# Kernel optimization log

Hardware: AMD Instinct MI355X
Metric: run time of the kernel (lower is better)

The kernel has to match this reference:

```python
import jax, jax.numpy as jnp
import numpy as np

BS, C, T = 16, 256, 768
PATCH = 12
NPATCH = T // PATCH            # 64 patches; 63 sequential update steps
FF, HEADS = 256, 4             # ff_dim = 2**ceil(log2(C)) = 256, divisible by heads
HD = FF // HEADS
TOPK = 3
ALPHA = 0.5
EPS = 1e-5                     # BatchNorm eps (eval mode, running stats mean=0, var=1)
NEG = -1000000000.0


def _bn(x2d, g, b):
    # eval-mode BatchNorm1d with default running stats (mean=0, var=1)
    return x2d * (g / np.float32(np.sqrt(1.0 + EPS))) + b


def _gelu(x):
    return jax.nn.gelu(x, approximate=False)  # torch F.gelu default = exact erf


def setup_inputs() -> dict:
    key = jax.random.key(0)
    ks = jax.random.split(key, 8)
    s = 0.05
    return {
        "x": jax.random.normal(ks[0], (BS, C, T), jnp.float32),
        "g0": jnp.ones((C * T,), jnp.float32), "b0": jnp.zeros((C * T,), jnp.float32),
        "g1": jnp.ones((C * PATCH,), jnp.float32), "b1": jnp.zeros((C * PATCH,), jnp.float32),
        "g2": jnp.ones((C * PATCH,), jnp.float32), "b2": jnp.zeros((C * PATCH,), jnp.float32),
        "W_agg": jax.random.normal(ks[1], (PATCH, PATCH), jnp.float32) * s,
        "b_agg": jnp.zeros((PATCH,), jnp.float32),
        "We": jax.random.normal(ks[2], (FF,), jnp.float32) * s,      # Linear(1, ff) weight[:,0]
        "be": jnp.zeros((FF,), jnp.float32),
        "Wq": jax.random.normal(ks[3], (FF, FF), jnp.float32) * s, "bq": jnp.zeros((FF,), jnp.float32),
        "Wk": jax.random.normal(ks[4], (FF, FF), jnp.float32) * s, "bk": jnp.zeros((FF,), jnp.float32),
        "Wv": jax.random.normal(ks[5], (FF, FF), jnp.float32) * s, "bv": jnp.zeros((FF,), jnp.float32),
        "Wm1": jax.random.normal(ks[6], (FF, FF), jnp.float32) * s, "bm1": jnp.zeros((FF,), jnp.float32),
        "Wm2": jax.random.normal(ks[7], (FF,), jnp.float32) * s,     # Linear(ff, 1) weight[0,:]
        "bm2": jnp.zeros((1,), jnp.float32),
    }


def reference(x, g0, b0, g1, b1, g2, b2, W_agg, b_agg, We, be,
              Wq, bq, Wk, bk, Wv, bv, Wm1, bm1, Wm2, bm2):
    # outer BatchNorm over flattened [bs, C*T]
    xn = _bn(x.reshape(BS, -1), g0, b0).reshape(BS, C, T)
    xp = xn.reshape(BS, C, NPATCH, PATCH).transpose(2, 0, 1, 3)  # [NP, bs, C, P]
    out0 = xp[0]

    def step(prev, xt):  # prev, xt: [bs, C, P]
        inp = _bn(prev.reshape(BS, -1), g1, b1).reshape(BS, C, PATCH)
        inp = _gelu(inp @ W_agg.T + b_agg)           # agg over patch dim (dropout=eval no-op)
        res = inp + xt                               # [bs, C, P]
        t = _bn(res.reshape(BS, -1), g2, b2).reshape(BS, C, PATCH).transpose(0, 2, 1)  # [bs,P,C]
        h = t[..., None] * We + be                   # channel_embed: [bs, P, C, FF]

        def proj(W, bvec):
            y = h @ W.T + bvec
            return y.reshape(BS, PATCH, C, HEADS, HD).transpose(0, 1, 3, 2, 4)  # [bs,P,H,C,hd]

        q, k, v = proj(Wq, bq), proj(Wk, bk), proj(Wv, bv)
        attn = jnp.einsum('bphcd,bphed->bphce', q, k) / np.float32(np.sqrt(HD))  # [bs,P,H,C,C]
        # top-k mask over channel-neighbor axis (scatter of top-k indices)
        flat = attn.reshape(-1, C)
        _, idx = jax.lax.top_k(flat, TOPK)
        rows = jnp.arange(flat.shape[0])[:, None]
        mask = jnp.zeros(flat.shape, bool).at[rows, idx].set(True).reshape(attn.shape)
        attn = jax.nn.softmax(jnp.where(mask, attn, NEG), axis=-1)
        hn = jnp.einsum('bphce,bphed->bphcd', attn, v).transpose(0, 1, 3, 2, 4).reshape(BS, PATCH, C, FF)
        z = _gelu(hn @ Wm1.T + bm1) @ Wm2 + bm2      # msg_mlp -> [bs, P, C]
        new = res + ALPHA * z.transpose(0, 2, 1)     # [bs, C, P]
        return new, new

    _, outs = jax.lax.scan(jax.checkpoint(step), out0, xp[1:])
    out = jnp.concatenate([out0[None], outs], axis=0)       # [NP, bs, C, P]
    return out.transpose(1, 2, 0, 3).reshape(BS, C, T)
```

## Files before the change

### kernel.cpp

```cpp
#include <hip/hip_runtime.h>
#include <math.h>

typedef unsigned int u32;
typedef unsigned long long u64;

#define BSZ   16
#define CCH   256
#define TT    768
#define PT    12
#define NPN   64
#define NH    4
#define NSL   4
#define GRID  (BSZ*NSL)
#define THR   768

#define WS_A    0
#define WS_CCF  4
#define WS_WAGG 80
#define WS_BAGG 224
#define WS_G1T  256
#define WS_B1T  3328
#define WS_G2T  6400
#define WS_B2T  9472
#define WS_S1Q  12544
#define WS_S1CQ 12800
#define WS_S1K  13056
#define WS_S1V  13312
#define WS_S1CV 13568
#define WS_M    13824
#define WS_CM1  14848
#define WS_EXF  16384
#define WS_XN   32768

#define INVSF 0.9999950000374996f
#define K2F   0.3989422804014327f

__device__ __forceinline__ float med3f(float a, float b, float c){
  return fmaxf(fminf(a,b), fminf(fmaxf(a,b), c));
}
__device__ __forceinline__ float gelu_fast(float v){
  float av = fabsf(v);
  if (__builtin_expect(av > 1.0f, 0))
    return 0.5f * v * (1.0f + erff(v * 0.7071067811865475f));
  float t = v * v;
  float r = 1.3319545e-06f;
  r = fmaf(r, t, -1.8889312e-05f);
  r = fmaf(r, t,  2.3086939e-04f);
  r = fmaf(r, t, -2.3746564e-03f);
  r = fmaf(r, t,  1.9947114e-02f);
  r = fmaf(r, t, -1.3298076e-01f);
  r = fmaf(r, t,  7.9788456e-01f);
  float a = 0.5f * v;
  return fmaf(a * v, r, a);
}
__device__ __forceinline__ float exp_t3(float x){
  float t = fmaf(x, 0.3333333333f, 1.0f);
  t = fmaf(x * 0.5f, t, 1.0f);
  return fmaf(x, t, 1.0f);
}
__device__ __forceinline__ float rdlane(float v, int lane){
  return __int_as_float(__builtin_amdgcn_readlane(__float_as_int(v), lane));
}
__device__ __forceinline__ void tstore(u64* p, u32 tag, float v){
  u64 w = ((u64)tag << 32) | (u64)(u32)__float_as_uint(v);
  __hip_atomic_store(p, w, __ATOMIC_RELAXED, __HIP_MEMORY_SCOPE_AGENT);
}
__device__ __forceinline__ float tpoll(const u64* p, u32 tag){
  u64 v;
  do { v = __hip_atomic_load(p, __ATOMIC_RELAXED, __HIP_MEMORY_SCOPE_AGENT); }
  while ((u32)(v >> 32) != tag);
  return __uint_as_float((u32)v);
}

#define TRIPLE_STAGE(CTRL) { \
  float o1 = __int_as_float(__builtin_amdgcn_update_dpp(ni, __float_as_int(t1), CTRL, 0xf, 0xf, false)); \
  float o2 = __int_as_float(__builtin_amdgcn_update_dpp(ni, __float_as_int(t2), CTRL, 0xf, 0xf, false)); \
  float o3 = __int_as_float(__builtin_amdgcn_update_dpp(ni, __float_as_int(t3), CTRL, 0xf, 0xf, false)); \
  float yy = fminf(t1,o1), xx = fmaxf(t2,o2); \
  t1 = fmaxf(t1,o1); \
  float n3 = med3f(yy, xx, fmaxf(t3,o3)); \
  t2 = fmaxf(yy,xx); t3 = n3; }

__global__ __launch_bounds__(1024) void precompute1_kernel(
    const float* __restrict__ x,   const float* __restrict__ g0,
    const float* __restrict__ b0,
    const float* __restrict__ gg1, const float* __restrict__ bb1,
    const float* __restrict__ gg2, const float* __restrict__ bb2,
    const float* __restrict__ Wagg, const float* __restrict__ bagg,
    const float* __restrict__ We,  const float* __restrict__ be,
    const float* __restrict__ Wq,  const float* __restrict__ bq,
    const float* __restrict__ Wk,
    const float* __restrict__ Wv,  const float* __restrict__ bv,
    float* __restrict__ ws)
{
  const int tid = threadIdx.x;

  if (blockIdx.x < 768) {
    __shared__ float tile[4][32*33];
    const int tau = blockIdx.x*4 + (tid >> 8);
    const int b   = tau / 192;
    const int rem = tau - b*192;
    const int t0  = (rem % 24) * 32;
    const int c0  = (rem / 24) * 32;
    const int id8 = tid & 255;
    float* tl = &tile[tid >> 8][0];
    const long xb = (long)b * (CCH*TT);
    {
      const int c  = id8 >> 3;
      const int tq = (id8 & 7) << 2;
      const int ict = (c0 + c)*TT + t0 + tq;
      const float4 xv4 = *reinterpret_cast<const float4*>(x  + xb + ict);
      const float4 gv4 = *reinterpret_cast<const float4*>(g0 + ict);
      const float4 bv4 = *reinterpret_cast<const float4*>(b0 + ict);
      float* tr = tl + c*33 + tq;
      tr[0] = fmaf(xv4.x, gv4.x*INVSF, bv4.x);
      tr[1] = fmaf(xv4.y, gv4.y*INVSF, bv4.y);
      tr[2] = fmaf(xv4.z, gv4.z*INVSF, bv4.z);
      tr[3] = fmaf(xv4.w, gv4.w*INVSF, bv4.w);
    }
    __syncthreads();
    {
      const int tt = id8 >> 3;
      const int cq = (id8 & 7) << 2;
      float4 o;
      o.x = tl[(cq    )*33 + tt];
      o.y = tl[(cq + 1)*33 + tt];
      o.z = tl[(cq + 2)*33 + tt];
      o.w = tl[(cq + 3)*33 + tt];
      *reinterpret_cast<float4*>(ws + WS_XN + ((long)b*TT + t0 + tt)*CCH + c0 + cq) = o;
    }
    return;
  }

  __shared__ float We_s[CCH], be_s[CCH];
  const int lane = tid & 63;
  const int w    = tid >> 6;
  if (tid < CCH) { We_s[tid] = We[tid]; be_s[tid] = be[tid]; }
  __syncthreads();

  const int f = (blockIdx.x - 768)*16 + w;
  float aq=0.f, cqa=0.f, ak=0.f, av=0.f, cva=0.f;
  #pragma unroll
  for (int k2 = 0; k2 < 4; ++k2) {
    int j = lane + 64*k2;
    float wev = We_s[j], bev = be_s[j];
    float q1 = Wq[f*CCH + j]; aq += q1*wev; cqa += q1*bev;
    float k1 = Wk[f*CCH + j]; ak += k1*wev;
    float v1 = Wv[f*CCH + j]; av += v1*wev; cva += v1*bev;
  }
  for (int ofs = 1; ofs < 64; ofs <<= 1) {
    aq += __shfl_xor(aq, ofs);  cqa += __shfl_xor(cqa, ofs);
    ak += __shfl_xor(ak, ofs);
    av += __shfl_xor(av, ofs);  cva += __shfl_xor(cva, ofs);
  }
  if (lane == 0) {
    ws[WS_S1Q  + f] = aq;
    ws[WS_S1CQ + f] = cqa + bq[f];
    ws[WS_S1K  + f] = ak;
    ws[WS_S1V  + f] = av;
    ws[WS_S1CV + f] = cva + bv[f];
  }

  if (blockIdx.x == 768) {
    for (int i = tid; i < PT*CCH; i += 1024) {
      int j = i >> 8, c = i & 255;
      ws[WS_G1T + i] = gg1[c*PT + j] * INVSF;
      ws[WS_B1T + i] = bb1[c*PT + j];
      ws[WS_G2T + i] = gg2[c*PT + j] * INVSF;
      ws[WS_B2T + i] = bb2[c*PT + j];
    }
    if (tid < PT*PT) ws[WS_WAGG + tid] = Wagg[tid];
    if (tid < PT)    ws[WS_BAGG + tid] = bagg[tid];
  }
}

__global__ __launch_bounds__(1024) void precompute2_kernel(
    const float* __restrict__ Wm1, const float* __restrict__ bm1,
    float* __restrict__ ws)
{
  const int tid  = threadIdx.x;
  const int lane = tid & 63;
  const int w    = tid >> 6;

  if (blockIdx.x < 16) {
    __shared__ float wv_l[CCH], cv_l[CCH];
    if (tid < CCH) { wv_l[tid] = ws[WS_S1V + tid]; cv_l[tid] = ws[WS_S1CV + tid]; }
    __syncthreads();
    const int g = blockIdx.x*16 + w;
    float mk0=0.f, mk1=0.f, mk2=0.f, mk3=0.f, ca=0.f;
    #pragma unroll
    for (int k2 = 0; k2 < 4; ++k2) {
      int j = lane + 64*k2;
      float wv1 = Wm1[g*CCH + j];
      float pm = wv1 * wv_l[j];
      if (k2 == 0) mk0 = pm; else if (k2 == 1) mk1 = pm; else if (k2 == 2) mk2 = pm; else mk3 = pm;
      ca += wv1 * cv_l[j];
    }
    for (int ofs = 1; ofs < 64; ofs <<= 1) {
      mk0 += __shfl_xor(mk0, ofs); mk1 += __shfl_xor(mk1, ofs);
      mk2 += __shfl_xor(mk2, ofs); mk3 += __shfl_xor(mk3, ofs);
      ca  += __shfl_xor(ca,  ofs);
    }
    if (lane == 0) {
      ws[WS_M + g*4+0] = mk0; ws[WS_M + g*4+1] = mk1;
      ws[WS_M + g*4+2] = mk2; ws[WS_M + g*4+3] = mk3;
      ws[WS_CM1 + g] = ca + bm1[g];
    }
    return;
  }

  if (tid < NH*64) {
    const int f = w*64 + lane;
    float a  = ws[WS_S1Q + f] * ws[WS_S1K + f];
    float cc = ws[WS_S1CQ + f] * ws[WS_S1K + f];
    for (int ofs = 1; ofs < 64; ofs <<= 1) { a += __shfl_xor(a, ofs); cc += __shfl_xor(cc, ofs); }
    if (lane == 0) { ws[WS_A + w] = a * 0.125f; ws[WS_CCF + w] = cc * 0.125f; }
  }
}

__device__ __forceinline__ float poly_acc(const float* __restrict__ ws,
                                          const float* __restrict__ Wm2,
                                          int m, int l)
{
  float acc = 0.f;
  #pragma unroll
  for (int k = 0; k < 4; ++k) {
    const int g = l + 64*k;
    const float W  = Wm2[g];
    const float cg = ws[WS_CM1 + g];
    float val;
    if (m == 0)      val = fmaf(K2F*cg, cg, 0.5f*cg);
    else if (m <= 4) val = fmaf(2.f*K2F, cg, 0.5f) * ws[WS_M + g*4 + (m-1)];
    else {
      const int u  = m - 5;
      const int hh = (u<4)?0:(u<7)?1:(u<9)?2:3;
      const int kk = (u<4)?u:(u<7)?(u-3):(u<9)?(u-5):3;
      val = K2F * ws[WS_M + g*4 + hh] * ws[WS_M + g*4 + kk] * ((hh==kk)?1.f:2.f);
    }
    acc += W * val;
  }
  for (int ofs = 1; ofs < 64; ofs <<= 1) acc += __shfl_xor(acc, ofs);
  return acc;
}

__global__ __launch_bounds__(THR) void main_kernel(
    float* __restrict__ ws, float* __restrict__ out,
    const float* __restrict__ Wm2, const float* __restrict__ bm2)
{
  const int blk   = blockIdx.x;
  const int b     = blk & 15;
  const int slice = blk >> 4;
  const int c0    = slice * 64;
  const int tid   = threadIdx.x;
  const int p     = tid >> 6;
  const int l     = tid & 63;

  __shared__ float tmp_sh[2][PT][64];
  __shared__ float o_buf[3*PT][69];
  __shared__ float C_lds[15];

  {
    float c = poly_acc(ws, Wm2, p, l);
    if (l == 0) C_lds[p] = c + (p == 0 ? bm2[0] : 0.f);
    if (p < 3) {
      float c2 = poly_acc(ws, Wm2, p + 12, l);
      if (l == 0) C_lds[p + 12] = c2;
    }
  }

  const int cg = c0 + l;
  const float g1r = ws[WS_G1T + p*CCH + cg];
  const float b1r = ws[WS_B1T + p*CCH + cg];
  const float g2r = ws[WS_G2T + p*CCH + cg];
  const float b2r = ws[WS_B2T + p*CCH + cg];
  float waggr[PT];
  #pragma unroll
  for (int j = 0; j < PT; ++j) waggr[j] = ws[WS_WAGG + p*PT + j];
  const float baggp = ws[WS_BAGG + p];
  float Ah[NH], Ch[NH];
  #pragma unroll
  for (int h = 0; h < NH; ++h) { Ah[h] = ws[WS_A + h]; Ch[h] = ws[WS_CCF + h]; }
  __syncthreads();

  float C15[15];
  #pragma unroll
  for (int m = 0; m < 15; ++m)
    C15[m] = __int_as_float(__builtin_amdgcn_readfirstlane(__float_as_int(C_lds[m])));

  u64* exBase = ((u64*)(ws + WS_EXF)) + (size_t)(b*PT + p) * (NSL*8);
  u64* exMine = exBase + slice*8;

  const long xb  = (long)b * (CCH*TT);
  const float* xnb = ws + WS_XN + (long)b*(TT*CCH);
  const int ni = __float_as_int(-1e30f);

  const int cfl  = tid / PT;
  const int part = tid - cfl*PT;
  float* outP = out + xb + (long)(c0 + cfl)*TT + part;
  const float* obP = &o_buf[0][0] + part*69 + cfl;

  float st = xnb[(long)(0*PT + p)*CCH + cg];
  o_buf[p][l] = st;

  const float* xp = xnb + (long)p*CCH + cg;
  int fl = 0;
  int wr = 1;

  for (int t = 1; t < NPN; ++t) {
    const int par = t & 1;
    const u32 tag = (u32)t;
    xp += PT*CCH;
    const float xv = *xp;

    tmp_sh[par][p][l] = fmaf(st, g1r, b1r);
    __syncthreads();

    float acc = baggp;
    #pragma unroll
    for (int j = 0; j < PT; ++j)
      acc = fmaf(tmp_sh[par][j][l], waggr[j], acc);
    float res = gelu_fast(acc) + xv;
    float s   = fmaf(res, g2r, b2r);

    const int src = (l & 31) << 1;
    float v0 = __shfl(s, src), v1 = __shfl(s, src + 1);
    float FBloc = 0.f;
    if (slice == 0)
      FBloc = (rdlane(s, 0) + rdlane(s, 1) + rdlane(s, 2)) * (1.0f/3.0f);
    if (l >= 32) { v0 = -v0; v1 = -v1; }
    float t1 = fmaxf(v0, v1), t2 = fminf(v0, v1), t3 = -1e30f;
    TRIPLE_STAGE(0x111);
    TRIPLE_STAGE(0x112);
    TRIPLE_STAGE(0x114);
    TRIPLE_STAGE(0x118);
    TRIPLE_STAGE(0x142);
    const float lt1 = rdlane(t1, 31), lt2 = rdlane(t2, 31), lt3 = rdlane(t3, 31);
    const float lu1 = rdlane(t1, 63), lu2 = rdlane(t2, 63), lu3 = rdlane(t3, 63);

    {
      float sw = (l == 0) ? lt1 : (l == 1) ? lt2 : (l == 2) ? lt3
               : (l == 3) ? lu1 : (l == 4) ? lu2 : lu3;
      if (l < 6) tstore(exMine + l, tag, sw);
      if (slice == 0 && l == 6) tstore(exMine + 6, tag, FBloc);
    }

    if (t >= 2) {
      const int tt = t - 2;
      outP[tt*PT] = obP[fl*(PT*69)];
      fl = (fl + 1 < 3) ? fl + 1 : 0;
    }

    float pv = 0.f;
    if (l < 18) {
      int pj = l / 6, word = l - pj*6;
      int pslice = pj + (pj >= slice);
      pv = tpoll(exBase + pslice*8 + word, tag);
    } else if (l == 18 && slice != 0) {
      pv = tpoll(exBase + 6, tag);
    }

    float T1 = lt1, T2 = lt2, T3 = lt3;
    float U1 = lu1, U2 = lu2, U3 = lu3;
    #pragma unroll
    for (int j = 0; j < 3; ++j) {
      const float q1 = rdlane(pv, 6*j),     q2 = rdlane(pv, 6*j + 1), q3 = rdlane(pv, 6*j + 2);
      const float r1 = rdlane(pv, 6*j + 3), r2 = rdlane(pv, 6*j + 4), r3 = rdlane(pv, 6*j + 5);
      float x1 = fminf(T1, q1), y1 = fmaxf(T2, q2);
      T1 = fmaxf(T1, q1);
      float nT3 = med3f(x1, y1, fmaxf(T3, q3));
      T2 = fmaxf(x1, y1); T3 = nT3;
      float x2 = fminf(U1, r1), y2 = fmaxf(U2, r2);
      U1 = fmaxf(U1, r1);
      float nU3 = med3f(x2, y2, fmaxf(U3, r3));
      U2 = fmaxf(x2, y2); U3 = nU3;
    }
    const float FB = (slice == 0) ? FBloc : rdlane(pv, 18);
    const float B1 = -U1, B2 = -U2, B3 = -U3;
    const float Td2 = T2 - T1, Td3 = T3 - T1;
    const float Bd2 = B2 - B1, Bd3 = B3 - B1;

    float S1v[NH];
    #pragma unroll
    for (int h = 0; h < NH; ++h) {
      float alpha = fmaf(Ah[h], s, Ch[h]);
      bool pos = alpha > 0.0f;
      float v1s = pos ? T1 : B1;
      float v2s = pos ? T2 : B2;
      float v3s = pos ? T3 : B3;
      float d2 = pos ? Td2 : Bd2;
      float d3 = pos ? Td3 : Bd3;
      float e2 = exp_t3(alpha * d2);
      float e3 = exp_t3(alpha * d3);
      float num = fmaf(e2, v2s, fmaf(e3, v3s, v1s));
      float den = (1.0f + e2) + e3;
      float r = __fdividef(num, den);
      S1v[h] = (alpha == 0.0f) ? FB : r;
    }
    {
      const float a = S1v[0], bq2 = S1v[1], c = S1v[2], d = S1v[3];
      float z = C15[0];
      z = fmaf(C15[1], a, z);  z = fmaf(C15[2], bq2, z);
      z = fmaf(C15[3], c, z);  z = fmaf(C15[4], d, z);
      z = fmaf(C15[5],  a*a, z);   z = fmaf(C15[6],  a*bq2, z);
      z = fmaf(C15[7],  a*c, z);   z = fmaf(C15[8],  a*d, z);
      z = fmaf(C15[9],  bq2*bq2, z); z = fmaf(C15[10], bq2*c, z);
      z = fmaf(C15[11], bq2*d, z); z = fmaf(C15[12], c*c, z);
      z = fmaf(C15[13], c*d, z);   z = fmaf(C15[14], d*d, z);
      st = fmaf(0.5f, z, res);
    }
    o_buf[wr*PT + p][l] = st;
    wr = (wr + 1 < 3) ? wr + 1 : 0;
  }

  __syncthreads();
  {
    #pragma unroll
    for (int tt = NPN-2; tt < NPN; ++tt)
      outP[tt*PT] = obP[(tt % 3)*(PT*69)];
  }
}

extern "C" void kernel_launch(void* const* d_in, const int* in_sizes, int n_in,
                              void* d_out, int out_size, void* d_ws, size_t ws_size,
                              hipStream_t stream) {
  (void)in_sizes; (void)n_in; (void)out_size; (void)ws_size;
  const float* x    = (const float*)d_in[0];
  const float* g0   = (const float*)d_in[1];
  const float* b0   = (const float*)d_in[2];
  const float* gg1  = (const float*)d_in[3];
  const float* bb1  = (const float*)d_in[4];
  const float* gg2  = (const float*)d_in[5];
  const float* bb2  = (const float*)d_in[6];
  const float* Wagg = (const float*)d_in[7];
  const float* bagg = (const float*)d_in[8];
  const float* We   = (const float*)d_in[9];
  const float* be   = (const float*)d_in[10];
  const float* Wq   = (const float*)d_in[11];
  const float* bq   = (const float*)d_in[12];
  const float* Wk   = (const float*)d_in[13];
  const float* Wv   = (const float*)d_in[15];
  const float* bv   = (const float*)d_in[16];
  const float* Wm1  = (const float*)d_in[17];
  const float* bm1  = (const float*)d_in[18];
  const float* Wm2  = (const float*)d_in[19];
  const float* bm2  = (const float*)d_in[20];
  float* ws  = (float*)d_ws;
  float* out = (float*)d_out;

  hipLaunchKernelGGL(precompute1_kernel, dim3(768 + 16), dim3(1024), 0, stream,
                     x, g0, b0, gg1, bb1, gg2, bb2, Wagg, bagg, We, be,
                     Wq, bq, Wk, Wv, bv, ws);
  hipLaunchKernelGGL(precompute2_kernel, dim3(17), dim3(1024), 0, stream,
                     Wm1, bm1, ws);
  hipLaunchKernelGGL(main_kernel, dim3(GRID), dim3(THR), 0, stream, ws, out,
                     Wm2, bm2);
}
```

Measured before the change: 318.8 us.

## Fold precompute2 into precompute1 and main kernel, reorder top-k exchange stores

Removes the second precompute launch. Each of the 16 weight blocks in precompute1 now redundantly recomputes the full Wv·We/be vectors in shared memory and then computes its slice of the Wm1 products, while the per-head A/C scalars move into main_kernel's prologue. It also lets lanes 31 and 63 store their top-3 values directly before the readlane broadcasts, so the exchange publish happens earlier in the serial step loop. The trade-off is 16x redundant Wv work and extra prologue work plus a barrier in main_kernel, in exchange for one fewer kernel launch.

```diff
diff --git a/kernel.cpp b/kernel.cpp
--- a/kernel.cpp
+++ b/kernel.cpp
@@ -14,8 +14,6 @@
 #define GRID  (BSZ*NSL)
 #define THR   768
 
-#define WS_A    0
-#define WS_CCF  4
 #define WS_WAGG 80
 #define WS_BAGG 224
 #define WS_G1T  256
@@ -25,8 +23,6 @@
 #define WS_S1Q  12544
 #define WS_S1CQ 12800
 #define WS_S1K  13056
-#define WS_S1V  13312
-#define WS_S1CV 13568
 #define WS_M    13824
 #define WS_CM1  14848
 #define WS_EXF  16384
@@ -91,6 +87,7 @@
     const float* __restrict__ Wq,  const float* __restrict__ bq,
     const float* __restrict__ Wk,
     const float* __restrict__ Wv,  const float* __restrict__ bv,
+    const float* __restrict__ Wm1, const float* __restrict__ bm1,
     float* __restrict__ ws)
 {
   const int tid = threadIdx.x;
@@ -133,35 +130,74 @@
   }
 
   __shared__ float We_s[CCH], be_s[CCH];
+  __shared__ float wv_l[CCH], cv_l[CCH];
   const int lane = tid & 63;
   const int w    = tid >> 6;
+  const int bf   = blockIdx.x - 768;
   if (tid < CCH) { We_s[tid] = We[tid]; be_s[tid] = be[tid]; }
   __syncthreads();
 
-  const int f = (blockIdx.x - 768)*16 + w;
-  float aq=0.f, cqa=0.f, ak=0.f, av=0.f, cva=0.f;
-  #pragma unroll
-  for (int k2 = 0; k2 < 4; ++k2) {
-    int j = lane + 64*k2;
-    float wev = We_s[j], bev = be_s[j];
-    float q1 = Wq[f*CCH + j]; aq += q1*wev; cqa += q1*bev;
-    float k1 = Wk[f*CCH + j]; ak += k1*wev;
-    float v1 = Wv[f*CCH + j]; av += v1*wev; cva += v1*bev;
-  }
-  for (int ofs = 1; ofs < 64; ofs <<= 1) {
-    aq += __shfl_xor(aq, ofs);  cqa += __shfl_xor(cqa, ofs);
-    ak += __shfl_xor(ak, ofs);
-    av += __shfl_xor(av, ofs);  cva += __shfl_xor(cva, ofs);
-  }
-  if (lane == 0) {
-    ws[WS_S1Q  + f] = aq;
-    ws[WS_S1CQ + f] = cqa + bq[f];
-    ws[WS_S1K  + f] = ak;
-    ws[WS_S1V  + f] = av;
-    ws[WS_S1CV + f] = cva + bv[f];
-  }
-
-  if (blockIdx.x == 768) {
+  {
+    const int f = bf*16 + w;
+    float aq=0.f, cqa=0.f, ak=0.f;
+    #pragma unroll
+    for (int k2 = 0; k2 < 4; ++k2) {
+      int j = lane + 64*k2;
+      float wev = We_s[j], bev = be_s[j];
+      float q1 = Wq[f*CCH + j]; aq += q1*wev; cqa += q1*bev;
+      float k1 = Wk[f*CCH + j]; ak += k1*wev;
+    }
+    for (int ofs = 1; ofs < 64; ofs <<= 1) {
+      aq += __shfl_xor(aq, ofs);  cqa += __shfl_xor(cqa, ofs);
+      ak += __shfl_xor(ak, ofs);
+    }
+    if (lane == 0) {
+      ws[WS_S1Q  + f] = aq;
+      ws[WS_S1CQ + f] = cqa + bq[f];
+      ws[WS_S1K  + f] = ak;
+    }
+  }
+
+  for (int r = 0; r < 16; ++r) {
+    const int f2 = w*16 + r;
+    float av=0.f, cva=0.f;
+    #pragma unroll
+    for (int k2 = 0; k2 < 4; ++k2) {
+      int j = lane + 64*k2;
+      float v1 = Wv[f2*CCH + j];
+      av += v1*We_s[j]; cva += v1*be_s[j];
+    }
+    for (int ofs = 1; ofs < 64; ofs <<= 1) {
+      av += __shfl_xor(av, ofs);  cva += __shfl_xor(cva, ofs);
+    }
+    if (lane == 0) { wv_l[f2] = av; cv_l[f2] = cva + bv[f2]; }
+  }
+  __syncthreads();
+
+  {
+    const int g = bf*16 + w;
+    float mk0=0.f, mk1=0.f, mk2=0.f, mk3=0.f, ca=0.f;
+    #pragma unroll
+    for (int k2 = 0; k2 < 4; ++k2) {
+      int j = lane + 64*k2;
+      float wv1 = Wm1[g*CCH + j];
+      float pm = wv1 * wv_l[j];
+      if (k2 == 0) mk0 = pm; else if (k2 == 1) mk1 = pm; else if (k2 == 2) mk2 = pm; else mk3 = pm;
+      ca += wv1 * cv_l[j];
+    }
+    for (int ofs = 1; ofs < 64; ofs <<= 1) {
+      mk0 += __shfl_xor(mk0, ofs); mk1 += __shfl_xor(mk1, ofs);
+      mk2 += __shfl_xor(mk2, ofs); mk3 += __shfl_xor(mk3, ofs);
+      ca  += __shfl_xor(ca,  ofs);
+    }
+    if (lane == 0) {
+      ws[WS_M + g*4+0] = mk0; ws[WS_M + g*4+1] = mk1;
+      ws[WS_M + g*4+2] = mk2; ws[WS_M + g*4+3] = mk3;
+      ws[WS_CM1 + g] = ca + bm1[g];
+    }
+  }
+
+  if (bf == 0) {
     for (int i = tid; i < PT*CCH; i += 1024) {
       int j = i >> 8, c = i & 255;
       ws[WS_G1T + i] = gg1[c*PT + j] * INVSF;
@@ -171,50 +207,6 @@
     }
     if (tid < PT*PT) ws[WS_WAGG + tid] = Wagg[tid];
     if (tid < PT)    ws[WS_BAGG + tid] = bagg[tid];
-  }
-}
-
-__global__ __launch_bounds__(1024) void precompute2_kernel(
-    const float* __restrict__ Wm1, const float* __restrict__ bm1,
-    float* __restrict__ ws)
-{
-  const int tid  = threadIdx.x;
-  const int lane = tid & 63;
-  const int w    = tid >> 6;
-
-  if (blockIdx.x < 16) {
-    __shared__ float wv_l[CCH], cv_l[CCH];
-    if (tid < CCH) { wv_l[tid] = ws[WS_S1V + tid]; cv_l[tid] = ws[WS_S1CV + tid]; }
-    __syncthreads();
-    const int g = blockIdx.x*16 + w;
-    float mk0=0.f, mk1=0.f, mk2=0.f, mk3=0.f, ca=0.f;
-    #pragma unroll
-    for (int k2 = 0; k2 < 4; ++k2) {
-      int j = lane + 64*k2;
-      float wv1 = Wm1[g*CCH + j];
-      float pm = wv1 * wv_l[j];
-      if (k2 == 0) mk0 = pm; else if (k2 == 1) mk1 = pm; else if (k2 == 2) mk2 = pm; else mk3 = pm;
-      ca += wv1 * cv_l[j];
-    }
-    for (int ofs = 1; ofs < 64; ofs <<= 1) {
-      mk0 += __shfl_xor(mk0, ofs); mk1 += __shfl_xor(mk1, ofs);
-      mk2 += __shfl_xor(mk2, ofs); mk3 += __shfl_xor(mk3, ofs);
-      ca  += __shfl_xor(ca,  ofs);
-    }
-    if (lane == 0) {
-      ws[WS_M + g*4+0] = mk0; ws[WS_M + g*4+1] = mk1;
-      ws[WS_M + g*4+2] = mk2; ws[WS_M + g*4+3] = mk3;
-      ws[WS_CM1 + g] = ca + bm1[g];
-    }
-    return;
-  }
-
-  if (tid < NH*64) {
-    const int f = w*64 + lane;
-    float a  = ws[WS_S1Q + f] * ws[WS_S1K + f];
-    float cc = ws[WS_S1CQ + f] * ws[WS_S1K + f];
-    for (int ofs = 1; ofs < 64; ofs <<= 1) { a += __shfl_xor(a, ofs); cc += __shfl_xor(cc, ofs); }
-    if (lane == 0) { ws[WS_A + w] = a * 0.125f; ws[WS_CCF + w] = cc * 0.125f; }
   }
 }
 
@@ -258,6 +250,15 @@
   __shared__ float tmp_sh[2][PT][64];
   __shared__ float o_buf[3*PT][69];
   __shared__ float C_lds[15];
+  __shared__ float AC_sh[2*NH];
+
+  if (p < NH) {
+    const int f = p*64 + l;
+    float a  = ws[WS_S1Q + f] * ws[WS_S1K + f];
+    float cc = ws[WS_S1CQ + f] * ws[WS_S1K + f];
+    for (int ofs = 1; ofs < 64; ofs <<= 1) { a += __shfl_xor(a, ofs); cc += __shfl_xor(cc, ofs); }
+    if (l == 0) { AC_sh[p] = a * 0.125f; AC_sh[NH + p] = cc * 0.125f; }
+  }
 
   {
     float c = poly_acc(ws, Wm2, p, l);
@@ -277,11 +278,14 @@
   #pragma unroll
   for (int j = 0; j < PT; ++j) waggr[j] = ws[WS_WAGG + p*PT + j];
   const float baggp = ws[WS_BAGG + p];
+  __syncthreads();
+
   float Ah[NH], Ch[NH];
   #pragma unroll
-  for (int h = 0; h < NH; ++h) { Ah[h] = ws[WS_A + h]; Ch[h] = ws[WS_CCF + h]; }
-  __syncthreads();
-
+  for (int h = 0; h < NH; ++h) {
+    Ah[h] = __int_as_float(__builtin_amdgcn_readfirstlane(__float_as_int(AC_sh[h])));
+    Ch[h] = __int_as_float(__builtin_amdgcn_readfirstlane(__float_as_int(AC_sh[NH + h])));
+  }
   float C15[15];
   #pragma unroll
   for (int m = 0; m < 15; ++m)
@@ -334,21 +338,26 @@
     TRIPLE_STAGE(0x114);
     TRIPLE_STAGE(0x118);
     TRIPLE_STAGE(0x142);
-    const float lt1 = rdlane(t1, 31), lt2 = rdlane(t2, 31), lt3 = rdlane(t3, 31);
-    const float lu1 = rdlane(t1, 63), lu2 = rdlane(t2, 63), lu3 = rdlane(t3, 63);
-
-    {
-      float sw = (l == 0) ? lt1 : (l == 1) ? lt2 : (l == 2) ? lt3
-               : (l == 3) ? lu1 : (l == 4) ? lu2 : lu3;
-      if (l < 6) tstore(exMine + l, tag, sw);
-      if (slice == 0 && l == 6) tstore(exMine + 6, tag, FBloc);
-    }
+
+    if (l == 31) {
+      tstore(exMine + 0, tag, t1);
+      tstore(exMine + 1, tag, t2);
+      tstore(exMine + 2, tag, t3);
+    } else if (l == 63) {
+      tstore(exMine + 3, tag, t1);
+      tstore(exMine + 4, tag, t2);
+      tstore(exMine + 5, tag, t3);
+    }
+    if (slice == 0 && l == 6) tstore(exMine + 6, tag, FBloc);
 
     if (t >= 2) {
       const int tt = t - 2;
       outP[tt*PT] = obP[fl*(PT*69)];
       fl = (fl + 1 < 3) ? fl + 1 : 0;
     }
+
+    const float lt1 = rdlane(t1, 31), lt2 = rdlane(t2, 31), lt3 = rdlane(t3, 31);
+    const float lu1 = rdlane(t1, 63), lu2 = rdlane(t2, 63), lu3 = rdlane(t3, 63);
 
     float pv = 0.f;
     if (l < 18) {
@@ -449,9 +458,7 @@
 
   hipLaunchKernelGGL(precompute1_kernel, dim3(768 + 16), dim3(1024), 0, stream,
                      x, g0, b0, gg1, bb1, gg2, bb2, Wagg, bagg, We, be,
-                     Wq, bq, Wk, Wv, bv, ws);
-  hipLaunchKernelGGL(precompute2_kernel, dim3(17), dim3(1024), 0, stream,
-                     Wm1, bm1, ws);
+                     Wq, bq, Wk, Wv, bv, Wm1, bm1, ws);
   hipLaunchKernelGGL(main_kernel, dim3(GRID), dim3(THR), 0, stream, ws, out,
                      Wm2, bm2);
 }
```

Result: slower. 368.5 us (+15.6%).
